# Optimization experiments

Measured on AMD Instinct MI355X. Metric: run time of the kernel, lower is better.

## Reference

```python
import jax, jax.numpy as jnp
import numpy as np

B, N, D, H = 8, 1024, 1024, 16
P = D // H
FACTOR = 1.0 / np.sqrt(P)
DFF = 4 * D


def layernorm(x, g, b, eps=1e-5):
    mu = jnp.mean(x, axis=-1, keepdims=True)
    var = jnp.var(x, axis=-1, keepdims=True)
    return (x - mu) * jax.lax.rsqrt(var + eps) * g + b


def setup_inputs() -> dict:
    key = jax.random.key(0)
    ks = jax.random.split(key, 6)
    s = 0.02
    return {
        "x": jax.random.normal(ks[0], (B, N, D), jnp.float32),
        "prior_attn": jax.random.normal(ks[1], (B, N, N), jnp.float32),
        "Wqkv": jax.random.normal(ks[2], (D, 3 * D), jnp.float32) * s,
        "bqkv": jnp.zeros((3 * D,), jnp.float32),
        "alpha": jnp.asarray(1.0, jnp.float32),
        "ln1_g": jnp.ones((D,), jnp.float32),
        "ln1_b": jnp.zeros((D,), jnp.float32),
        "ln2_g": jnp.ones((D,), jnp.float32),
        "ln2_b": jnp.zeros((D,), jnp.float32),
        "w1": jax.random.normal(ks[3], (D, DFF), jnp.float32) * s,
        "b1": jnp.zeros((DFF,), jnp.float32),
        "w2": jax.random.normal(ks[4], (DFF, D), jnp.float32) * s,
        "b2": jnp.zeros((D,), jnp.float32),
    }


def reference(x, prior_attn, Wqkv, bqkv, alpha, ln1_g, ln1_b, ln2_g, ln2_b, w1, b1, w2, b2):
    b, n, d = x.shape
    # --- PriorMSA on ln_1(x) ---
    z1 = layernorm(x, ln1_g, ln1_b)
    qkv = z1 @ Wqkv + bqkv                      # [b, n, 3d]
    q, k, v = jnp.split(qkv, 3, axis=-1)
    q = q.reshape(b, n, H, P)
    k = k.reshape(b, n, H, P)
    v = v.reshape(b, n, H, P)
    raw = jnp.einsum('bihp,bjhp->bhij', q, k)   # [b, h, n, n]
    raw = raw + alpha * prior_attn[:, None, :, :]
    attn = jax.nn.softmax(raw * FACTOR, axis=-1)
    out = jnp.einsum('bhij,bjhp->bihp', attn, v).reshape(b, n, d)
    s1 = x + out                                 # residual (no out-projection in source)
    # --- MLP on ln_2(s1) ---
    z2 = layernorm(s1, ln2_g, ln2_b)
    mlp = jax.nn.gelu(z2 @ w1 + b1) @ w2 + b2
    return s1 + mlp
```

## Files before the change

### kernel.cpp

```cpp
#include <hip/hip_runtime.h>
#include <hip/hip_bf16.h>
#include <stdint.h>


typedef __attribute__((ext_vector_type(8))) short short8;
typedef __attribute__((ext_vector_type(4))) float f32x4;

__device__ __forceinline__ int is_bf16_in(const void* ln1g) {
  return *(const uint32_t*)ln1g == 0x3F803F80u;
}
__device__ __forceinline__ float bf2f(uint16_t u) {
  union { uint32_t i; float f; } v; v.i = ((uint32_t)u) << 16; return v.f;
}
__device__ __forceinline__ uint16_t f2bf(float f) {
  union { float f; uint32_t i; } v; v.f = f;
  uint32_t r = v.i + 0x7FFFu + ((v.i >> 16) & 1u);
  return (uint16_t)(r >> 16);
}
__device__ __forceinline__ float ldin(const void* p, size_t i, int bf) {
  return bf ? bf2f(((const uint16_t*)p)[i]) : ((const float*)p)[i];
}
__device__ __forceinline__ uint32_t pack_bf(float a, float b) {
  union { float f; uint32_t u; } ua, ub; ua.f = a; ub.f = b;
  return ((ua.u + 0x8000u) >> 16) | ((ub.u + 0x8000u) & 0xFFFF0000u);
}

typedef __attribute__((address_space(1))) void gvoid;
typedef __attribute__((address_space(3))) void lvoid;
__device__ __forceinline__ void gld16(const uint16_t* g, uint16_t* l) {
  __builtin_amdgcn_global_load_lds((const gvoid*)g, (lvoid*)l, 16, 0, 0);
}

__device__ __forceinline__ float gelu_f(float x) {
  float u = 0.7978845608028654f * (x + 0.044715f * x * x * x);
  float e = __expf(-2.0f * fabsf(u));
  float t = (1.0f - e) / (1.0f + e);
  t = (u >= 0.f) ? t : -t;
  return 0.5f * x * (1.0f + t);
}

template<int EPI>
__global__ __launch_bounds__(256) void gemm_bt(
    const uint16_t* __restrict__ A, const uint16_t* __restrict__ Bt,
    const void* __restrict__ bias, const void* __restrict__ flagsrc,
    void* __restrict__ Cout, const float* __restrict__ resid,
    int M, int N, int K)
{
  __shared__ __align__(16) uint16_t As[4096];
  __shared__ __align__(16) uint16_t Bs[4096];
  const int t = threadIdx.x;
  const int wv = t >> 6;
  const int lane = t & 63;
  const int ln = lane & 15, quad = lane >> 4;
  const int wm = (wv & 1) * 64, wn = (wv >> 1) * 64;
  const int row0 = blockIdx.y * 128, col0 = blockIdx.x * 128;

  auto mk = [&](const uint16_t* Pb, int base, int c) -> const uint16_t* {
    int m = c >> 2, s = c & 3;
    int kc = s ^ (m & 3) ^ ((m >> 2) & 3);
    return Pb + (size_t)(base + m) * K + kc * 8;
  };
  const uint16_t* a0 = mk(A, row0, t);
  const uint16_t* a1 = mk(A, row0, t + 256);
  const uint16_t* b0 = mk(Bt, col0, t);
  const uint16_t* b1 = mk(Bt, col0, t + 256);
  uint16_t* lA0 = &As[(wv * 64) * 8];
  uint16_t* lA1 = &As[(256 + wv * 64) * 8];
  uint16_t* lB0 = &Bs[(wv * 64) * 8];
  uint16_t* lB1 = &Bs[(256 + wv * 64) * 8];

  int aidx[4], bidx[4];
#pragma unroll
  for (int i = 0; i < 4; ++i) {
    int m = wm + i * 16 + ln;
    aidx[i] = (m * 4 + (quad ^ (m & 3) ^ ((m >> 2) & 3))) * 8;
    int n = wn + i * 16 + ln;
    bidx[i] = (n * 4 + (quad ^ (n & 3) ^ ((n >> 2) & 3))) * 8;
  }

  f32x4 acc[4][4];
#pragma unroll
  for (int i = 0; i < 4; ++i)
#pragma unroll
    for (int j = 0; j < 4; ++j) acc[i][j] = (f32x4){0.f, 0.f, 0.f, 0.f};

  for (int kt = 0; kt < K; kt += 32) {
    __syncthreads();
    gld16(a0 + kt, lA0);
    gld16(a1 + kt, lA1);
    gld16(b0 + kt, lB0);
    gld16(b1 + kt, lB1);
    __syncthreads();
    short8 av[4], bv[4];
#pragma unroll
    for (int i = 0; i < 4; ++i) av[i] = *(const short8*)&As[aidx[i]];
#pragma unroll
    for (int i = 0; i < 4; ++i) bv[i] = *(const short8*)&Bs[bidx[i]];
#pragma unroll
    for (int i = 0; i < 4; ++i)
#pragma unroll
      for (int j = 0; j < 4; ++j)
        acc[i][j] = __builtin_amdgcn_mfma_f32_16x16x32_bf16(av[i], bv[j], acc[i][j], 0, 0, 0);
  }

  const int bf = is_bf16_in(flagsrc);
#pragma unroll
  for (int i = 0; i < 4; ++i) {
#pragma unroll
    for (int j = 0; j < 4; ++j) {
#pragma unroll
      for (int r = 0; r < 4; ++r) {
        int gr = row0 + wm + i * 16 + quad * 4 + r;
        int gc = col0 + wn + j * 16 + ln;
        float v = acc[i][j][r] + ldin(bias, gc, bf);
        size_t oi = (size_t)gr * N + gc;
        if (EPI == 0)      ((uint16_t*)Cout)[oi] = f2bf(v);
        else if (EPI == 1) ((uint16_t*)Cout)[oi] = f2bf(gelu_f(v));
        else               ((float*)Cout)[oi] = v + resid[oi];
      }
    }
  }
}

__global__ __launch_bounds__(256) void ln_rows(
    const void* __restrict__ in, int in_f32ws,
    const void* __restrict__ g_, const void* __restrict__ b_,
    uint16_t* __restrict__ out, const void* __restrict__ flagsrc)
{
  const int row = blockIdx.x;
  const int t = threadIdx.x;
  const int bf = is_bf16_in(flagsrc);
  size_t base = (size_t)row * 1024;
  float v[4];
  if (in_f32ws || !bf) {
    f32x4 vv = *(const f32x4*)((const float*)in + base + t * 4);
    v[0] = vv[0]; v[1] = vv[1]; v[2] = vv[2]; v[3] = vv[3];
  } else {
    ushort4 u = *(const ushort4*)((const uint16_t*)in + base + t * 4);
    v[0] = bf2f(u.x); v[1] = bf2f(u.y); v[2] = bf2f(u.z); v[3] = bf2f(u.w);
  }
  float s = v[0] + v[1] + v[2] + v[3];
  float q = v[0]*v[0] + v[1]*v[1] + v[2]*v[2] + v[3]*v[3];
#pragma unroll
  for (int m = 1; m < 64; m <<= 1) {
    s += __shfl_xor(s, m);
    q += __shfl_xor(q, m);
  }
  __shared__ float red[8];
  if ((t & 63) == 0) { red[t >> 6] = s; red[4 + (t >> 6)] = q; }
  __syncthreads();
  s = red[0] + red[1] + red[2] + red[3];
  q = red[4] + red[5] + red[6] + red[7];
  float mu = s * (1.0f / 1024.0f);
  float var = q * (1.0f / 1024.0f) - mu * mu;
  float rs = rsqrtf(var + 1e-5f);
  int c = t * 4;
  float gg[4], bb[4];
  if (!bf) {
    f32x4 gv = *(const f32x4*)((const float*)g_ + c);
    f32x4 bv = *(const f32x4*)((const float*)b_ + c);
    gg[0]=gv[0]; gg[1]=gv[1]; gg[2]=gv[2]; gg[3]=gv[3];
    bb[0]=bv[0]; bb[1]=bv[1]; bb[2]=bv[2]; bb[3]=bv[3];
  } else {
    ushort4 gv = *(const ushort4*)((const uint16_t*)g_ + c);
    ushort4 bv = *(const ushort4*)((const uint16_t*)b_ + c);
    gg[0]=bf2f(gv.x); gg[1]=bf2f(gv.y); gg[2]=bf2f(gv.z); gg[3]=bf2f(gv.w);
    bb[0]=bf2f(bv.x); bb[1]=bf2f(bv.y); bb[2]=bf2f(bv.z); bb[3]=bf2f(bv.w);
  }
  ushort4 o;
  o.x = f2bf((v[0] - mu) * rs * gg[0] + bb[0]);
  o.y = f2bf((v[1] - mu) * rs * gg[1] + bb[1]);
  o.z = f2bf((v[2] - mu) * rs * gg[2] + bb[2]);
  o.w = f2bf((v[3] - mu) * rs * gg[3] + bb[3]);
  *(ushort4*)(out + base + c) = o;
}

__global__ __launch_bounds__(256) void transpose_w(
    const void* __restrict__ W, uint16_t* __restrict__ Wt,
    int Kd, int Nw, const void* __restrict__ flagsrc)
{
  __shared__ float T[64][65];
  const int bf = is_bf16_in(flagsrc);
  int n0 = blockIdx.x * 64, k0 = blockIdx.y * 64;
  int t = threadIdx.x;
#pragma unroll
  for (int it = 0; it < 16; ++it) {
    int idx = t + it * 256;
    int r = idx >> 6, c = idx & 63;
    T[r][c] = ldin(W, (size_t)(k0 + r) * Nw + n0 + c, bf);
  }
  __syncthreads();
#pragma unroll
  for (int it = 0; it < 16; ++it) {
    int idx = t + it * 256;
    int rr = idx >> 6, cc = idx & 63;
    Wt[(size_t)(n0 + rr) * Kd + k0 + cc] = f2bf(T[cc][rr]);
  }
}

__global__ __launch_bounds__(256) void transpose_v(
    const uint16_t* __restrict__ qkv, uint16_t* __restrict__ vT)
{
  __shared__ uint16_t T[64][65];
  int n0 = blockIdx.x * 64;
  int h = blockIdx.y, b = blockIdx.z;
  int t = threadIdx.x;
#pragma unroll
  for (int it = 0; it < 16; ++it) {
    int idx = t + it * 256;
    int r = idx >> 6, c = idx & 63;
    T[r][c] = qkv[(size_t)(b * 1024 + n0 + r) * 3072 + 2048 + h * 64 + c];
  }
  __syncthreads();
#pragma unroll
  for (int it = 0; it < 16; ++it) {
    int idx = t + it * 256;
    int rr = idx >> 6, cc = idx & 63;
    vT[(size_t)((b * 16 + h) * 64 + rr) * 1024 + n0 + cc] = T[cc][rr];
  }
}

__global__ __launch_bounds__(256, 4) void attn_fused2(
    const uint16_t* __restrict__ qkv, const uint16_t* __restrict__ vT,
    const void* __restrict__ prior, const void* __restrict__ x,
    const void* __restrict__ alpha_p, const void* __restrict__ flagsrc,
    float* __restrict__ s1)
{
  __shared__ __align__(16) uint16_t sm[3 * 4608];
  uint16_t* Qs = sm;
  uint16_t* Ks = sm + 4608;
  uint16_t* Vs = sm + 9216;
  uint16_t* Ss = sm;
  float* Obuf = (float*)(sm + 4608);

  const int t = threadIdx.x;
  const int w = t >> 6, lane = t & 63, ln = lane & 15, quad = lane >> 4;
  const int q0 = blockIdx.x * 64;
  const int h = blockIdx.y, b = blockIdx.z;
  const int bf = is_bf16_in(flagsrc);
  const float alpha = ldin(alpha_p, 0, bf);
  const float c1 = 0.125f * 1.44269504088896340736f;
  const float c2 = alpha * c1;

  const int r8 = t >> 3, c8 = t & 7;

  {
    const uint16_t* src = &qkv[(size_t)(b * 1024 + q0 + r8) * 3072 + h * 64 + c8 * 8];
    uint4 qa = *(const uint4*)src;
    uint4 qb = *(const uint4*)(src + (size_t)32 * 3072);
    *(uint4*)&Qs[r8 * 72 + c8 * 8] = qa;
    *(uint4*)&Qs[(r8 + 32) * 72 + c8 * 8] = qb;
  }
  const uint16_t* kbase = &qkv[(size_t)(b * 1024 + r8) * 3072 + 1024 + h * 64 + c8 * 8];
  const uint16_t* vbase = &vT[(size_t)((b * 16 + h) * 64 + r8) * 1024 + c8 * 8];
  uint4 kr0 = *(const uint4*)kbase;
  uint4 kr1 = *(const uint4*)(kbase + (size_t)32 * 3072);
  uint4 vr0 = *(const uint4*)vbase;
  uint4 vr1 = *(const uint4*)(vbase + (size_t)32 * 1024);
  __syncthreads();
  short8 qf0 = *(const short8*)&Qs[(16 * w + ln) * 72 + quad * 8];
  short8 qf1 = *(const short8*)&Qs[(16 * w + ln) * 72 + 32 + quad * 8];

  f32x4 o[4];
#pragma unroll
  for (int i = 0; i < 4; ++i) o[i] = (f32x4){0.f, 0.f, 0.f, 0.f};
  float accl = 0.f;

  for (int j = 0; j < 16; ++j) {
    __syncthreads();
    *(uint4*)&Ks[r8 * 72 + c8 * 8] = kr0;
    *(uint4*)&Ks[(r8 + 32) * 72 + c8 * 8] = kr1;
    *(uint4*)&Vs[r8 * 72 + c8 * 8] = vr0;
    *(uint4*)&Vs[(r8 + 32) * 72 + c8 * 8] = vr1;
    __syncthreads();
    if (j < 15) {
      const uint16_t* kp = kbase + (size_t)(j + 1) * 64 * 3072;
      kr0 = *(const uint4*)kp;
      kr1 = *(const uint4*)(kp + (size_t)32 * 3072);
      const uint16_t* vp = vbase + (j + 1) * 64;
      vr0 = *(const uint4*)vp;
      vr1 = *(const uint4*)(vp + (size_t)32 * 1024);
    }
    float pv[4][4];
    {
      size_t pri = ((size_t)(b * 1024 + q0 + 16 * w + ln)) * 1024 + j * 64 + 4 * quad;
      if (!bf) {
        const float* pb = (const float*)prior + pri;
#pragma unroll
        for (int nt = 0; nt < 4; ++nt) {
          f32x4 pp = *(const f32x4*)(pb + 16 * nt);
          pv[nt][0] = pp[0]; pv[nt][1] = pp[1]; pv[nt][2] = pp[2]; pv[nt][3] = pp[3];
        }
      } else {
        const uint16_t* pb = (const uint16_t*)prior + pri;
#pragma unroll
        for (int nt = 0; nt < 4; ++nt) {
          ushort4 pp = *(const ushort4*)(pb + 16 * nt);
          pv[nt][0] = bf2f(pp.x); pv[nt][1] = bf2f(pp.y);
          pv[nt][2] = bf2f(pp.z); pv[nt][3] = bf2f(pp.w);
        }
      }
    }
    f32x4 st[4];
#pragma unroll
    for (int nt = 0; nt < 4; ++nt) {
      short8 kf0 = *(const short8*)&Ks[(16 * nt + ln) * 72 + quad * 8];
      short8 kf1 = *(const short8*)&Ks[(16 * nt + ln) * 72 + 32 + quad * 8];
      f32x4 z = (f32x4){0.f, 0.f, 0.f, 0.f};
      z = __builtin_amdgcn_mfma_f32_16x16x32_bf16(kf0, qf0, z, 0, 0, 0);
      st[nt] = __builtin_amdgcn_mfma_f32_16x16x32_bf16(kf1, qf1, z, 0, 0, 0);
    }
    asm volatile("" ::: "memory");
#pragma unroll
    for (int nt = 0; nt < 4; ++nt) {
      float p0 = exp2f(st[nt][0] * c1 + pv[nt][0] * c2);
      float p1 = exp2f(st[nt][1] * c1 + pv[nt][1] * c2);
      float p2 = exp2f(st[nt][2] * c1 + pv[nt][2] * c2);
      float p3 = exp2f(st[nt][3] * c1 + pv[nt][3] * c2);
      accl += (p0 + p1) + (p2 + p3);
      uint2 pk;
      pk.x = pack_bf(p0, p1);
      pk.y = pack_bf(p2, p3);
      *(uint2*)&Ss[(16 * w + ln) * 72 + 16 * nt + 4 * quad] = pk;
    }
    asm volatile("" ::: "memory");
    short8 pf0 = *(const short8*)&Ss[(16 * w + ln) * 72 + quad * 8];
    short8 pf1 = *(const short8*)&Ss[(16 * w + ln) * 72 + 32 + quad * 8];
#pragma unroll
    for (int dt = 0; dt < 4; ++dt) {
      short8 vf0 = *(const short8*)&Vs[(16 * dt + ln) * 72 + quad * 8];
      short8 vf1 = *(const short8*)&Vs[(16 * dt + ln) * 72 + 32 + quad * 8];
      o[dt] = __builtin_amdgcn_mfma_f32_16x16x32_bf16(vf0, pf0, o[dt], 0, 0, 0);
      o[dt] = __builtin_amdgcn_mfma_f32_16x16x32_bf16(vf1, pf1, o[dt], 0, 0, 0);
    }
  }

  accl += __shfl_xor(accl, 16);
  accl += __shfl_xor(accl, 32);
  float inv = 1.0f / accl;

  __syncthreads();
#pragma unroll
  for (int dt = 0; dt < 4; ++dt) {
    f32x4 ov = o[dt] * inv;
    *(f32x4*)&Obuf[(16 * w + ln) * 68 + 16 * dt + 4 * quad] = ov;
  }
  __syncthreads();
  {
    int row = t >> 2, cc0 = (t & 3) * 16;
    size_t gbase = ((size_t)(b * 1024 + q0 + row)) * 1024 + h * 64 + cc0;
#pragma unroll
    for (int i = 0; i < 4; ++i) {
      f32x4 ov = *(const f32x4*)&Obuf[row * 68 + cc0 + 4 * i];
      f32x4 xr;
      if (!bf) {
        xr = *(const f32x4*)((const float*)x + gbase + 4 * i);
      } else {
        ushort4 xu = *(const ushort4*)((const uint16_t*)x + gbase + 4 * i);
        xr = (f32x4){bf2f(xu.x), bf2f(xu.y), bf2f(xu.z), bf2f(xu.w)};
      }
      *(f32x4*)(s1 + gbase + 4 * i) = ov + xr;
    }
  }
}

extern "C" void kernel_launch(void* const* d_in, const int* in_sizes, int n_in,
                              void* d_out, int out_size, void* d_ws, size_t ws_size,
                              hipStream_t stream)
{
  const void* x     = d_in[0];
  const void* prior = d_in[1];
  const void* Wqkv  = d_in[2];
  const void* bqkv  = d_in[3];
  const void* alpha = d_in[4];
  const void* ln1g  = d_in[5];
  const void* ln1b  = d_in[6];
  const void* ln2g  = d_in[7];
  const void* ln2b  = d_in[8];
  const void* w1    = d_in[9];
  const void* b1    = d_in[10];
  const void* w2    = d_in[11];
  const void* b2    = d_in[12];

  char* ws = (char*)d_ws;
  uint16_t* wqkvt = (uint16_t*)(ws + 256);
  uint16_t* w1t   = (uint16_t*)(ws + 6291712);
  uint16_t* w2t   = (uint16_t*)(ws + 14680320);
  uint16_t* z     = (uint16_t*)(ws + 23068928);
  uint16_t* qkv   = (uint16_t*)(ws + 39846144);
  uint16_t* vT    = (uint16_t*)(ws + 90177792);
  float*    s1    = (float*)(ws + 106955008);
  uint16_t* h1    = qkv;

  transpose_w<<<dim3(48, 16), 256, 0, stream>>>(Wqkv, wqkvt, 1024, 3072, ln1g);
  transpose_w<<<dim3(64, 16), 256, 0, stream>>>(w1, w1t, 1024, 4096, ln1g);
  transpose_w<<<dim3(16, 64), 256, 0, stream>>>(w2, w2t, 4096, 1024, ln1g);
  ln_rows<<<8192, 256, 0, stream>>>(x, 0, ln1g, ln1b, z, ln1g);
  gemm_bt<0><<<dim3(24, 64), 256, 0, stream>>>(z, wqkvt, bqkv, ln1g, qkv, nullptr, 8192, 3072, 1024);
  transpose_v<<<dim3(16, 16, 8), 256, 0, stream>>>(qkv, vT);
  attn_fused2<<<dim3(16, 16, 8), 256, 0, stream>>>(qkv, vT, prior, x, alpha, ln1g, s1);
  ln_rows<<<8192, 256, 0, stream>>>(s1, 1, ln2g, ln2b, z, ln1g);
  gemm_bt<1><<<dim3(32, 64), 256, 0, stream>>>(z, w1t, b1, ln1g, h1, nullptr, 8192, 4096, 1024);
  gemm_bt<2><<<dim3(8, 64), 256, 0, stream>>>(h1, w2t, b2, ln1g, d_out, s1, 8192, 1024, 4096);
}
```

Measured before the change: 627.1 us.

## Deepen GEMM K-tile, vectorize epilogues, pre-convert prior to bf16, double attention query tile

The GEMM now loads a 64-wide K slice per barrier pair instead of 32, using an 8-way XOR swizzle, and swaps the MFMA operand order so each lane holds four contiguous columns. That lets the epilogue write packed bf16 or float4 stores and read the bias as a vector. GELU is replaced by a sigmoid-form tanh approximation built on the hardware exp2 and rcp instructions. A new kernel converts prior_attn to bf16 once, so attention reads half the bytes, but this adds a pass and rounds the prior to bf16. The attention kernel now handles 128 query rows per block, two 16-row tiles per wave with Q kept in registers, so each K/V tile loaded into LDS is reused twice.

```diff
diff --git a/kernel.cpp b/kernel.cpp
--- a/kernel.cpp
+++ b/kernel.cpp
@@ -32,11 +32,10 @@
 }
 
 __device__ __forceinline__ float gelu_f(float x) {
-  float u = 0.7978845608028654f * (x + 0.044715f * x * x * x);
-  float e = __expf(-2.0f * fabsf(u));
-  float t = (1.0f - e) / (1.0f + e);
-  t = (u >= 0.f) ? t : -t;
-  return 0.5f * x * (1.0f + t);
+  float t1 = x * x;
+  float s = fmaf(t1, -0.1029498f, -2.3023457f);
+  float e = __builtin_amdgcn_exp2f(x * s);
+  return x * __builtin_amdgcn_rcpf(1.0f + e);
 }
 
 template<int EPI>
@@ -46,8 +45,8 @@
     void* __restrict__ Cout, const float* __restrict__ resid,
     int M, int N, int K)
 {
-  __shared__ __align__(16) uint16_t As[4096];
-  __shared__ __align__(16) uint16_t Bs[4096];
+  __shared__ __align__(16) uint16_t As[8192];
+  __shared__ __align__(16) uint16_t Bs[8192];
   const int t = threadIdx.x;
   const int wv = t >> 6;
   const int lane = t & 63;
@@ -56,26 +55,32 @@
   const int row0 = blockIdx.y * 128, col0 = blockIdx.x * 128;
 
   auto mk = [&](const uint16_t* Pb, int base, int c) -> const uint16_t* {
-    int m = c >> 2, s = c & 3;
-    int kc = s ^ (m & 3) ^ ((m >> 2) & 3);
+    int m = c >> 3, s = c & 7;
+    int kc = s ^ (m & 7);
     return Pb + (size_t)(base + m) * K + kc * 8;
   };
-  const uint16_t* a0 = mk(A, row0, t);
-  const uint16_t* a1 = mk(A, row0, t + 256);
-  const uint16_t* b0 = mk(Bt, col0, t);
-  const uint16_t* b1 = mk(Bt, col0, t + 256);
-  uint16_t* lA0 = &As[(wv * 64) * 8];
-  uint16_t* lA1 = &As[(256 + wv * 64) * 8];
-  uint16_t* lB0 = &Bs[(wv * 64) * 8];
-  uint16_t* lB1 = &Bs[(256 + wv * 64) * 8];
-
-  int aidx[4], bidx[4];
-#pragma unroll
-  for (int i = 0; i < 4; ++i) {
-    int m = wm + i * 16 + ln;
-    aidx[i] = (m * 4 + (quad ^ (m & 3) ^ ((m >> 2) & 3))) * 8;
-    int n = wn + i * 16 + ln;
-    bidx[i] = (n * 4 + (quad ^ (n & 3) ^ ((n >> 2) & 3))) * 8;
+  const uint16_t* ap[4];
+  const uint16_t* bp[4];
+  uint16_t* lA[4];
+  uint16_t* lB[4];
+#pragma unroll
+  for (int q = 0; q < 4; ++q) {
+    ap[q] = mk(A, row0, t + q * 256);
+    bp[q] = mk(Bt, col0, t + q * 256);
+    lA[q] = &As[(q * 256 + wv * 64) * 8];
+    lB[q] = &Bs[(q * 256 + wv * 64) * 8];
+  }
+
+  int aidx[2][4], bidx[2][4];
+#pragma unroll
+  for (int kh = 0; kh < 2; ++kh) {
+#pragma unroll
+    for (int i = 0; i < 4; ++i) {
+      int m = wm + i * 16 + ln;
+      aidx[kh][i] = (m * 8 + ((kh * 4 + quad) ^ (m & 7))) * 8;
+      int n = wn + i * 16 + ln;
+      bidx[kh][i] = (n * 8 + ((kh * 4 + quad) ^ (n & 7))) * 8;
+    }
   }
 
   f32x4 acc[4][4];
@@ -84,39 +89,59 @@
 #pragma unroll
     for (int j = 0; j < 4; ++j) acc[i][j] = (f32x4){0.f, 0.f, 0.f, 0.f};
 
-  for (int kt = 0; kt < K; kt += 32) {
+  for (int kt = 0; kt < K; kt += 64) {
     __syncthreads();
-    gld16(a0 + kt, lA0);
-    gld16(a1 + kt, lA1);
-    gld16(b0 + kt, lB0);
-    gld16(b1 + kt, lB1);
+#pragma unroll
+    for (int q = 0; q < 4; ++q) gld16(ap[q] + kt, lA[q]);
+#pragma unroll
+    for (int q = 0; q < 4; ++q) gld16(bp[q] + kt, lB[q]);
     __syncthreads();
-    short8 av[4], bv[4];
-#pragma unroll
-    for (int i = 0; i < 4; ++i) av[i] = *(const short8*)&As[aidx[i]];
-#pragma unroll
-    for (int i = 0; i < 4; ++i) bv[i] = *(const short8*)&Bs[bidx[i]];
-#pragma unroll
-    for (int i = 0; i < 4; ++i)
-#pragma unroll
-      for (int j = 0; j < 4; ++j)
-        acc[i][j] = __builtin_amdgcn_mfma_f32_16x16x32_bf16(av[i], bv[j], acc[i][j], 0, 0, 0);
+#pragma unroll
+    for (int kh = 0; kh < 2; ++kh) {
+      short8 av[4], bv[4];
+#pragma unroll
+      for (int i = 0; i < 4; ++i) av[i] = *(const short8*)&As[aidx[kh][i]];
+#pragma unroll
+      for (int j = 0; j < 4; ++j) bv[j] = *(const short8*)&Bs[bidx[kh][j]];
+#pragma unroll
+      for (int i = 0; i < 4; ++i)
+#pragma unroll
+        for (int j = 0; j < 4; ++j)
+          acc[i][j] = __builtin_amdgcn_mfma_f32_16x16x32_bf16(bv[j], av[i], acc[i][j], 0, 0, 0);
+    }
   }
 
   const int bf = is_bf16_in(flagsrc);
 #pragma unroll
-  for (int i = 0; i < 4; ++i) {
-#pragma unroll
-    for (int j = 0; j < 4; ++j) {
-#pragma unroll
-      for (int r = 0; r < 4; ++r) {
-        int gr = row0 + wm + i * 16 + quad * 4 + r;
-        int gc = col0 + wn + j * 16 + ln;
-        float v = acc[i][j][r] + ldin(bias, gc, bf);
-        size_t oi = (size_t)gr * N + gc;
-        if (EPI == 0)      ((uint16_t*)Cout)[oi] = f2bf(v);
-        else if (EPI == 1) ((uint16_t*)Cout)[oi] = f2bf(gelu_f(v));
-        else               ((float*)Cout)[oi] = v + resid[oi];
+  for (int j = 0; j < 4; ++j) {
+    int gc0 = col0 + wn + j * 16 + quad * 4;
+    float bs[4];
+    if (!bf) {
+      f32x4 bv4 = *(const f32x4*)((const float*)bias + gc0);
+      bs[0] = bv4[0]; bs[1] = bv4[1]; bs[2] = bv4[2]; bs[3] = bv4[3];
+    } else {
+      ushort4 bu = *(const ushort4*)((const uint16_t*)bias + gc0);
+      bs[0] = bf2f(bu.x); bs[1] = bf2f(bu.y); bs[2] = bf2f(bu.z); bs[3] = bf2f(bu.w);
+    }
+#pragma unroll
+    for (int i = 0; i < 4; ++i) {
+      int gr = row0 + wm + i * 16 + ln;
+      size_t oi = (size_t)gr * N + gc0;
+      float v0 = acc[i][j][0] + bs[0];
+      float v1 = acc[i][j][1] + bs[1];
+      float v2 = acc[i][j][2] + bs[2];
+      float v3 = acc[i][j][3] + bs[3];
+      if (EPI == 0) {
+        uint2 pk; pk.x = pack_bf(v0, v1); pk.y = pack_bf(v2, v3);
+        *(uint2*)((uint16_t*)Cout + oi) = pk;
+      } else if (EPI == 1) {
+        v0 = gelu_f(v0); v1 = gelu_f(v1); v2 = gelu_f(v2); v3 = gelu_f(v3);
+        uint2 pk; pk.x = pack_bf(v0, v1); pk.y = pack_bf(v2, v3);
+        *(uint2*)((uint16_t*)Cout + oi) = pk;
+      } else {
+        f32x4 rv = *(const f32x4*)(resid + oi);
+        f32x4 ov = (f32x4){v0 + rv[0], v1 + rv[1], v2 + rv[2], v3 + rv[3]};
+        *(f32x4*)((float*)Cout + oi) = ov;
       }
     }
   }
@@ -167,12 +192,10 @@
     gg[0]=bf2f(gv.x); gg[1]=bf2f(gv.y); gg[2]=bf2f(gv.z); gg[3]=bf2f(gv.w);
     bb[0]=bf2f(bv.x); bb[1]=bf2f(bv.y); bb[2]=bf2f(bv.z); bb[3]=bf2f(bv.w);
   }
-  ushort4 o;
-  o.x = f2bf((v[0] - mu) * rs * gg[0] + bb[0]);
-  o.y = f2bf((v[1] - mu) * rs * gg[1] + bb[1]);
-  o.z = f2bf((v[2] - mu) * rs * gg[2] + bb[2]);
-  o.w = f2bf((v[3] - mu) * rs * gg[3] + bb[3]);
-  *(ushort4*)(out + base + c) = o;
+  uint2 o;
+  o.x = pack_bf((v[0] - mu) * rs * gg[0] + bb[0], (v[1] - mu) * rs * gg[1] + bb[1]);
+  o.y = pack_bf((v[2] - mu) * rs * gg[2] + bb[2], (v[3] - mu) * rs * gg[3] + bb[3]);
+  *(uint2*)(out + base + c) = o;
 }
 
 __global__ __launch_bounds__(256) void transpose_w(
@@ -220,51 +243,64 @@
   }
 }
 
-__global__ __launch_bounds__(256, 4) void attn_fused2(
+__global__ __launch_bounds__(256) void prior_cvt(
+    const void* __restrict__ prior, uint16_t* __restrict__ out,
+    const void* __restrict__ flagsrc)
+{
+  const int bf = is_bf16_in(flagsrc);
+  size_t i = ((size_t)blockIdx.x * 256 + threadIdx.x) * 4;
+  if (bf) {
+    *(ushort4*)(out + i) = *(const ushort4*)((const uint16_t*)prior + i);
+  } else {
+    f32x4 v = *(const f32x4*)((const float*)prior + i);
+    uint2 pk; pk.x = pack_bf(v[0], v[1]); pk.y = pack_bf(v[2], v[3]);
+    *(uint2*)(out + i) = pk;
+  }
+}
+
+__global__ __launch_bounds__(256) void attn_fused3(
     const uint16_t* __restrict__ qkv, const uint16_t* __restrict__ vT,
-    const void* __restrict__ prior, const void* __restrict__ x,
+    const uint16_t* __restrict__ priorb, const void* __restrict__ x,
     const void* __restrict__ alpha_p, const void* __restrict__ flagsrc,
     float* __restrict__ s1)
 {
-  __shared__ __align__(16) uint16_t sm[3 * 4608];
-  uint16_t* Qs = sm;
-  uint16_t* Ks = sm + 4608;
-  uint16_t* Vs = sm + 9216;
-  uint16_t* Ss = sm;
-  float* Obuf = (float*)(sm + 4608);
+  __shared__ __align__(16) uint16_t sm[18432];
+  uint16_t* Ks = sm;
+  uint16_t* Vs = sm + 4608;
+  uint16_t* Ss = sm + 9216;
+  float* Obuf = (float*)sm;
 
   const int t = threadIdx.x;
   const int w = t >> 6, lane = t & 63, ln = lane & 15, quad = lane >> 4;
-  const int q0 = blockIdx.x * 64;
+  const int q0 = blockIdx.x * 128;
   const int h = blockIdx.y, b = blockIdx.z;
   const int bf = is_bf16_in(flagsrc);
   const float alpha = ldin(alpha_p, 0, bf);
   const float c1 = 0.125f * 1.44269504088896340736f;
   const float c2 = alpha * c1;
+  uint16_t* Ssw = Ss + w * 2304;
 
   const int r8 = t >> 3, c8 = t & 7;
 
-  {
-    const uint16_t* src = &qkv[(size_t)(b * 1024 + q0 + r8) * 3072 + h * 64 + c8 * 8];
-    uint4 qa = *(const uint4*)src;
-    uint4 qb = *(const uint4*)(src + (size_t)32 * 3072);
-    *(uint4*)&Qs[r8 * 72 + c8 * 8] = qa;
-    *(uint4*)&Qs[(r8 + 32) * 72 + c8 * 8] = qb;
-  }
+  short8 qf[2][2];
+#pragma unroll
+  for (int qt = 0; qt < 2; ++qt) {
+    const uint16_t* qsrc = &qkv[(size_t)(b * 1024 + q0 + 32 * w + 16 * qt + ln) * 3072 + h * 64 + quad * 8];
+    qf[qt][0] = *(const short8*)qsrc;
+    qf[qt][1] = *(const short8*)(qsrc + 32);
+  }
+
   const uint16_t* kbase = &qkv[(size_t)(b * 1024 + r8) * 3072 + 1024 + h * 64 + c8 * 8];
   const uint16_t* vbase = &vT[(size_t)((b * 16 + h) * 64 + r8) * 1024 + c8 * 8];
   uint4 kr0 = *(const uint4*)kbase;
   uint4 kr1 = *(const uint4*)(kbase + (size_t)32 * 3072);
   uint4 vr0 = *(const uint4*)vbase;
   uint4 vr1 = *(const uint4*)(vbase + (size_t)32 * 1024);
-  __syncthreads();
-  short8 qf0 = *(const short8*)&Qs[(16 * w + ln) * 72 + quad * 8];
-  short8 qf1 = *(const short8*)&Qs[(16 * w + ln) * 72 + 32 + quad * 8];
-
-  f32x4 o[4];
-#pragma unroll
-  for (int i = 0; i < 4; ++i) o[i] = (f32x4){0.f, 0.f, 0.f, 0.f};
-  float accl = 0.f;
+
+  f32x4 o[4][2];
+#pragma unroll
+  for (int i = 0; i < 4; ++i) { o[i][0] = (f32x4){0.f,0.f,0.f,0.f}; o[i][1] = (f32x4){0.f,0.f,0.f,0.f}; }
+  float accl[2] = {0.f, 0.f};
 
   for (int j = 0; j < 16; ++j) {
     __syncthreads();
@@ -281,73 +317,71 @@
       vr0 = *(const uint4*)vp;
       vr1 = *(const uint4*)(vp + (size_t)32 * 1024);
     }
-    float pv[4][4];
-    {
-      size_t pri = ((size_t)(b * 1024 + q0 + 16 * w + ln)) * 1024 + j * 64 + 4 * quad;
-      if (!bf) {
-        const float* pb = (const float*)prior + pri;
-#pragma unroll
-        for (int nt = 0; nt < 4; ++nt) {
-          f32x4 pp = *(const f32x4*)(pb + 16 * nt);
-          pv[nt][0] = pp[0]; pv[nt][1] = pp[1]; pv[nt][2] = pp[2]; pv[nt][3] = pp[3];
-        }
-      } else {
-        const uint16_t* pb = (const uint16_t*)prior + pri;
-#pragma unroll
-        for (int nt = 0; nt < 4; ++nt) {
-          ushort4 pp = *(const ushort4*)(pb + 16 * nt);
-          pv[nt][0] = bf2f(pp.x); pv[nt][1] = bf2f(pp.y);
-          pv[nt][2] = bf2f(pp.z); pv[nt][3] = bf2f(pp.w);
-        }
-      }
-    }
-    f32x4 st[4];
+    ushort4 pv[2][4];
+#pragma unroll
+    for (int qt = 0; qt < 2; ++qt) {
+      const uint16_t* pb = priorb + ((size_t)(b * 1024 + q0 + 32 * w + 16 * qt + ln)) * 1024 + j * 64 + 4 * quad;
+#pragma unroll
+      for (int nt = 0; nt < 4; ++nt) pv[qt][nt] = *(const ushort4*)(pb + 16 * nt);
+    }
 #pragma unroll
     for (int nt = 0; nt < 4; ++nt) {
       short8 kf0 = *(const short8*)&Ks[(16 * nt + ln) * 72 + quad * 8];
       short8 kf1 = *(const short8*)&Ks[(16 * nt + ln) * 72 + 32 + quad * 8];
-      f32x4 z = (f32x4){0.f, 0.f, 0.f, 0.f};
-      z = __builtin_amdgcn_mfma_f32_16x16x32_bf16(kf0, qf0, z, 0, 0, 0);
-      st[nt] = __builtin_amdgcn_mfma_f32_16x16x32_bf16(kf1, qf1, z, 0, 0, 0);
+#pragma unroll
+      for (int qt = 0; qt < 2; ++qt) {
+        f32x4 z = (f32x4){0.f, 0.f, 0.f, 0.f};
+        z = __builtin_amdgcn_mfma_f32_16x16x32_bf16(kf0, qf[qt][0], z, 0, 0, 0);
+        z = __builtin_amdgcn_mfma_f32_16x16x32_bf16(kf1, qf[qt][1], z, 0, 0, 0);
+        float p0 = __builtin_amdgcn_exp2f(z[0] * c1 + bf2f(pv[qt][nt].x) * c2);
+        float p1 = __builtin_amdgcn_exp2f(z[1] * c1 + bf2f(pv[qt][nt].y) * c2);
+        float p2 = __builtin_amdgcn_exp2f(z[2] * c1 + bf2f(pv[qt][nt].z) * c2);
+        float p3 = __builtin_amdgcn_exp2f(z[3] * c1 + bf2f(pv[qt][nt].w) * c2);
+        accl[qt] += (p0 + p1) + (p2 + p3);
+        uint2 pk; pk.x = pack_bf(p0, p1); pk.y = pack_bf(p2, p3);
+        *(uint2*)&Ssw[(16 * qt + ln) * 72 + 16 * nt + 4 * quad] = pk;
+      }
     }
     asm volatile("" ::: "memory");
-#pragma unroll
-    for (int nt = 0; nt < 4; ++nt) {
-      float p0 = exp2f(st[nt][0] * c1 + pv[nt][0] * c2);
-      float p1 = exp2f(st[nt][1] * c1 + pv[nt][1] * c2);
-      float p2 = exp2f(st[nt][2] * c1 + pv[nt][2] * c2);
-      float p3 = exp2f(st[nt][3] * c1 + pv[nt][3] * c2);
-      accl += (p0 + p1) + (p2 + p3);
-      uint2 pk;
-      pk.x = pack_bf(p0, p1);
-      pk.y = pack_bf(p2, p3);
-      *(uint2*)&Ss[(16 * w + ln) * 72 + 16 * nt + 4 * quad] = pk;
-    }
-    asm volatile("" ::: "memory");
-    short8 pf0 = *(const short8*)&Ss[(16 * w + ln) * 72 + quad * 8];
-    short8 pf1 = *(const short8*)&Ss[(16 * w + ln) * 72 + 32 + quad * 8];
+    short8 pf[2][2];
+#pragma unroll
+    for (int qt = 0; qt < 2; ++qt) {
+      pf[qt][0] = *(const short8*)&Ssw[(16 * qt + ln) * 72 + quad * 8];
+      pf[qt][1] = *(const short8*)&Ssw[(16 * qt + ln) * 72 + 32 + quad * 8];
+    }
 #pragma unroll
     for (int dt = 0; dt < 4; ++dt) {
       short8 vf0 = *(const short8*)&Vs[(16 * dt + ln) * 72 + quad * 8];
       short8 vf1 = *(const short8*)&Vs[(16 * dt + ln) * 72 + 32 + quad * 8];
-      o[dt] = __builtin_amdgcn_mfma_f32_16x16x32_bf16(vf0, pf0, o[dt], 0, 0, 0);
-      o[dt] = __builtin_amdgcn_mfma_f32_16x16x32_bf16(vf1, pf1, o[dt], 0, 0, 0);
-    }
-  }
-
-  accl += __shfl_xor(accl, 16);
-  accl += __shfl_xor(accl, 32);
-  float inv = 1.0f / accl;
+#pragma unroll
+      for (int qt = 0; qt < 2; ++qt) {
+        o[dt][qt] = __builtin_amdgcn_mfma_f32_16x16x32_bf16(vf0, pf[qt][0], o[dt][qt], 0, 0, 0);
+        o[dt][qt] = __builtin_amdgcn_mfma_f32_16x16x32_bf16(vf1, pf[qt][1], o[dt][qt], 0, 0, 0);
+      }
+    }
+  }
+
+  float inv[2];
+#pragma unroll
+  for (int qt = 0; qt < 2; ++qt) {
+    float a = accl[qt];
+    a += __shfl_xor(a, 16);
+    a += __shfl_xor(a, 32);
+    inv[qt] = 1.0f / a;
+  }
 
   __syncthreads();
 #pragma unroll
-  for (int dt = 0; dt < 4; ++dt) {
-    f32x4 ov = o[dt] * inv;
-    *(f32x4*)&Obuf[(16 * w + ln) * 68 + 16 * dt + 4 * quad] = ov;
-  }
+  for (int qt = 0; qt < 2; ++qt)
+#pragma unroll
+    for (int dt = 0; dt < 4; ++dt) {
+      f32x4 ov = o[dt][qt] * inv[qt];
+      *(f32x4*)&Obuf[(32 * w + 16 * qt + ln) * 68 + 16 * dt + 4 * quad] = ov;
+    }
   __syncthreads();
-  {
-    int row = t >> 2, cc0 = (t & 3) * 16;
+#pragma unroll
+  for (int half = 0; half < 2; ++half) {
+    int row = half * 64 + (t >> 2), cc0 = (t & 3) * 16;
     size_t gbase = ((size_t)(b * 1024 + q0 + row)) * 1024 + h * 64 + cc0;
 #pragma unroll
     for (int i = 0; i < 4; ++i) {
@@ -391,14 +425,16 @@
   uint16_t* vT    = (uint16_t*)(ws + 90177792);
   float*    s1    = (float*)(ws + 106955008);
   uint16_t* h1    = qkv;
+  uint16_t* priorb = z;
 
   transpose_w<<<dim3(48, 16), 256, 0, stream>>>(Wqkv, wqkvt, 1024, 3072, ln1g);
   transpose_w<<<dim3(64, 16), 256, 0, stream>>>(w1, w1t, 1024, 4096, ln1g);
   transpose_w<<<dim3(16, 64), 256, 0, stream>>>(w2, w2t, 4096, 1024, ln1g);
   ln_rows<<<8192, 256, 0, stream>>>(x, 0, ln1g, ln1b, z, ln1g);
   gemm_bt<0><<<dim3(24, 64), 256, 0, stream>>>(z, wqkvt, bqkv, ln1g, qkv, nullptr, 8192, 3072, 1024);
+  prior_cvt<<<8192, 256, 0, stream>>>(prior, priorb, ln1g);
   transpose_v<<<dim3(16, 16, 8), 256, 0, stream>>>(qkv, vT);
-  attn_fused2<<<dim3(16, 16, 8), 256, 0, stream>>>(qkv, vT, prior, x, alpha, ln1g, s1);
+  attn_fused3<<<dim3(8, 16, 8), 256, 0, stream>>>(qkv, vT, priorb, x, alpha, ln1g, s1);
   ln_rows<<<8192, 256, 0, stream>>>(s1, 1, ln2g, ln2b, z, ln1g);
   gemm_bt<1><<<dim3(32, 64), 256, 0, stream>>>(z, w1t, b1, ln1g, h1, nullptr, 8192, 4096, 1024);
   gemm_bt<2><<<dim3(8, 64), 256, 0, stream>>>(h1, w2t, b2, ln1g, d_out, s1, 8192, 1024, 4096);
```

Result: faster. 579.1 us (-7.7%).
